# Optimization experiments

Measured on AMD Instinct MI355X. Metric: run time of the kernel, lower is better.

The kernel has to match this reference:

```python
import jax, jax.numpy as jnp
import numpy as np

N_HEADS = 16
N_KV_HEADS = 4
HEAD_DIM = 128  # n_embd // n_head = 2048 // 16
NEG_INF = -1e9


def setup_inputs() -> dict:
    key = jax.random.key(0)
    ks = jax.random.split(key, 4)
    B, T, C = 8, 1024, 2048
    x = jax.random.normal(ks[0], (B, T, C), dtype=jnp.float32)
    sc = 1.0 / np.sqrt(C)
    Wq = jax.random.normal(ks[1], (C, C), dtype=jnp.float32) * sc
    bq = jnp.zeros((C,), dtype=jnp.float32)
    Wkv = jax.random.normal(ks[2], (N_KV_HEADS * HEAD_DIM * 2, C), dtype=jnp.float32) * sc
    bkv = jnp.zeros((N_KV_HEADS * HEAD_DIM * 2,), dtype=jnp.float32)
    Wo = jax.random.normal(ks[3], (C, C), dtype=jnp.float32) * sc
    bo = jnp.zeros((C,), dtype=jnp.float32)
    return {"x": x, "Wq": Wq, "bq": bq, "Wkv": Wkv, "bkv": bkv, "Wo": Wo, "bo": bo}


def reference(x, Wq, bq, Wkv, bkv, Wo, bo):
    B, T, C = x.shape
    g = N_HEADS // N_KV_HEADS  # group size for repeat_interleave
    # q: [B, H, T, D]
    q = (x @ Wq.T + bq).reshape(B, T, N_HEADS, HEAD_DIM).transpose(0, 2, 1, 3)
    # kv: [B, T, Hkv, 2, D] -> [B, Hkv, T, 2, D]
    kv = (x @ Wkv.T + bkv).reshape(B, T, N_KV_HEADS, 2, HEAD_DIM).transpose(0, 2, 1, 3, 4)
    k = kv[..., 0, :]  # [B, Hkv, T, D]
    v = kv[..., 1, :]
    # repeat_interleave along head dim to expand kv heads to full heads
    k = jnp.repeat(k, g, axis=1)  # [B, H, T, D]
    v = jnp.repeat(v, g, axis=1)
    scale = 1.0 / jnp.sqrt(jnp.asarray(HEAD_DIM, dtype=x.dtype))
    scores = jnp.einsum('bhqd,bhkd->bhqk', q, k) * scale  # [B, H, T, T]
    causal = jnp.tril(jnp.ones((T, T), dtype=bool))
    scores = jnp.where(causal[None, None], scores, NEG_INF)
    attn = jax.nn.softmax(scores, axis=-1)
    y = jnp.einsum('bhqk,bhkd->bhqd', attn, v)  # [B, H, T, D]
    y = y.transpose(0, 2, 1, 3).reshape(B, T, C)
    return y @ Wo.T + bo
```

## Files before the change

kernel.cpp:

```cpp
#include <hip/hip_runtime.h>

typedef short short8 __attribute__((ext_vector_type(8)));
typedef short short4v __attribute__((ext_vector_type(4)));
typedef float floatx4 __attribute__((ext_vector_type(4)));
typedef unsigned short ushort_t;
typedef unsigned int uint_t;

#define DI __device__ __forceinline__

DI ushort_t f2bf(float f) {
  uint_t u = __builtin_bit_cast(uint_t, f);
  uint_t r = u + 0x7FFFu + ((u >> 16) & 1u);
  return (ushort_t)(r >> 16);
}

DI float exp2a(float x) {
  float r;
  asm("v_exp_f32 %0, %1" : "=v"(r) : "v"(x));
  return r;
}

DI floatx4 mfma16(short8 a, short8 b, floatx4 c) {
  return __builtin_amdgcn_mfma_f32_16x16x32_bf16(a, b, c, 0, 0, 0);
}

DI void async16(const void* g, void* l) {
  __builtin_amdgcn_global_load_lds(
      (__attribute__((address_space(1))) void*)(g),
      (__attribute__((address_space(3))) void*)(l), 16, 0, 0);
}

DI void cfence() { asm volatile("" ::: "memory"); }

__global__ __launch_bounds__(256)
void k_f2bf4(const float* __restrict__ x, const float* __restrict__ wq,
             const float* __restrict__ wkv, const float* __restrict__ wo,
             ushort_t* __restrict__ xb, ushort_t* __restrict__ wqb,
             ushort_t* __restrict__ wkvb, ushort_t* __restrict__ wob)
{
  const int blk = blockIdx.x;
  const float* in; ushort_t* out; long base;
  if (blk < 8192)       { in = x;   out = xb;   base = (long)blk * 2048; }
  else if (blk < 10240) { in = wq;  out = wqb;  base = (long)(blk - 8192) * 2048; }
  else if (blk < 11264) { in = wkv; out = wkvb; base = (long)(blk - 10240) * 2048; }
  else                  { in = wo;  out = wob;  base = (long)(blk - 11264) * 2048; }
  const long i = base + (long)threadIdx.x * 8;
  const float4 a = *(const float4*)(in + i);
  const float4 b = *(const float4*)(in + i + 4);
  union { short8 s; ushort_t u[8]; } o;
  o.u[0] = f2bf(a.x); o.u[1] = f2bf(a.y); o.u[2] = f2bf(a.z); o.u[3] = f2bf(a.w);
  o.u[4] = f2bf(b.x); o.u[5] = f2bf(b.y); o.u[6] = f2bf(b.z); o.u[7] = f2bf(b.w);
  *(short8*)(out + i) = o.s;
}

__global__ __launch_bounds__(256)
void k_gemmkv(const ushort_t* __restrict__ A, const ushort_t* __restrict__ B,
              const float* __restrict__ bias, ushort_t* __restrict__ KVout,
              ushort_t* __restrict__ Vt, int N, int K)
{
  __shared__ __align__(16) ushort_t As[4][128 * 32];
  __shared__ __align__(16) ushort_t Bs[4][128 * 32];
  const int tid = threadIdx.x;
  const int w = tid >> 6, l = tid & 63;
  const int wm = w >> 1, wn = w & 1;
  const int lr = l & 15, lg = l >> 4;
  const long m0 = (long)blockIdx.y * 128;
  const long n0 = (long)blockIdx.x * 128;

  const floatx4 fz = {0.f, 0.f, 0.f, 0.f};
  floatx4 acc[4][4];
#pragma unroll
  for (int i = 0; i < 4; ++i)
#pragma unroll
    for (int j = 0; j < 4; ++j) acc[i][j] = fz;

  const int c0 = tid, c1 = 256 + tid;
  const int r0 = c0 >> 2, r1 = c1 >> 2;
  const ushort_t* gA0 = A + (m0 + r0) * K + (((c0 & 3) ^ (r0 & 3)) << 3);
  const ushort_t* gA1 = A + (m0 + r1) * K + (((c1 & 3) ^ (r1 & 3)) << 3);
  const ushort_t* gB0 = B + (n0 + r0) * K + (((c0 & 3) ^ (r0 & 3)) << 3);
  const ushort_t* gB1 = B + (n0 + r1) * K + (((c1 & 3) ^ (r1 & 3)) << 3);

  const int nK = K >> 5;
#pragma unroll
  for (int pt = 0; pt < 3; ++pt) {
    const int ko = pt << 5;
    async16(gA0 + ko, &As[pt][c0 * 8]);
    async16(gA1 + ko, &As[pt][c1 * 8]);
    async16(gB0 + ko, &Bs[pt][c0 * 8]);
    async16(gB1 + ko, &Bs[pt][c1 * 8]);
  }

  const int xg = (lr & 3);

  for (int kt = 0; kt < nK; ++kt) {
    const int cur = kt & 3;
    const int rem = nK - 1 - kt;
    if (rem >= 3) {
      const int ko = (kt + 3) << 5;
      const int nb = (kt + 3) & 3;
      async16(gA0 + ko, &As[nb][c0 * 8]);
      async16(gA1 + ko, &As[nb][c1 * 8]);
      async16(gB0 + ko, &Bs[nb][c0 * 8]);
      async16(gB1 + ko, &Bs[nb][c1 * 8]);
      asm volatile("s_waitcnt vmcnt(12)" ::: "memory");
    } else if (rem == 2) {
      asm volatile("s_waitcnt vmcnt(8)" ::: "memory");
    } else if (rem == 1) {
      asm volatile("s_waitcnt vmcnt(4)" ::: "memory");
    } else {
      asm volatile("s_waitcnt vmcnt(0)" ::: "memory");
    }
    __builtin_amdgcn_s_barrier();
    cfence();

    short8 a[4], b[4];
#pragma unroll
    for (int i = 0; i < 4; ++i)
      a[i] = *(const short8*)&As[cur][(wm * 64 + i * 16 + lr) * 32 + ((lg ^ xg) * 8)];
#pragma unroll
    for (int j = 0; j < 4; ++j)
      b[j] = *(const short8*)&Bs[cur][(wn * 64 + j * 16 + lr) * 32 + ((lg ^ xg) * 8)];
#pragma unroll
    for (int i = 0; i < 4; ++i)
#pragma unroll
      for (int j = 0; j < 4; ++j)
        acc[i][j] = mfma16(a[i], b[j], acc[i][j]);

    asm volatile("s_waitcnt lgkmcnt(0)" ::: "memory");
    __builtin_amdgcn_s_barrier();
    cfence();
  }

#pragma unroll
  for (int j = 0; j < 4; ++j) {
    const long gn = n0 + wn * 64 + j * 16 + lr;
    const float bv = bias[gn];
    const int isV = (int)((gn >> 7) & 1);
    const long vrowB = (long)((gn >> 8) * 128 + (gn & 127)) * 1024;
#pragma unroll
    for (int i = 0; i < 4; ++i) {
      const long gm = m0 + wm * 64 + i * 16 + lg * 4;
#pragma unroll
      for (int r = 0; r < 4; ++r) {
        const ushort_t ov = f2bf(acc[i][j][r] + bv);
        const long gmr = gm + r;
        if (isV) Vt[((gmr >> 10) * 512) * 1024 + vrowB + (gmr & 1023)] = ov;
        else     KVout[gmr * 1024 + gn] = ov;
      }
    }
  }
}

template<int OUT_BF16>
__global__ __launch_bounds__(512, 4)
void k_gemm3(const ushort_t* __restrict__ A, const ushort_t* __restrict__ B,
             const float* __restrict__ bias, void* __restrict__ Cout,
             int N, int K, int gx, float out_scale)
{
  __shared__ __align__(16) ushort_t Al[2][256 * 32];
  __shared__ __align__(16) ushort_t Bl[2][128 * 32];
  const int tid = threadIdx.x;
  const int w = tid >> 6, l = tid & 63;
  const int wr = w >> 1, wc = w & 1;
  const int lr = l & 15, lg = l >> 4;

  const int nwg = gridDim.x;
  const int qd = nwg >> 3;
  const int p = blockIdx.x;
  const int swz = (p & 7) * qd + (p >> 3);
  const long m0 = (long)(swz / gx) * 256;
  const long n0 = (long)(swz % gx) * 128;

  const floatx4 fz = {0.f, 0.f, 0.f, 0.f};
  floatx4 acc[4][4];
#pragma unroll
  for (int i = 0; i < 4; ++i)
#pragma unroll
    for (int j = 0; j < 4; ++j) acc[i][j] = fz;

  const int cA0 = tid, cA1 = 512 + tid, cB = tid;
  const int rA0 = cA0 >> 2, rA1 = cA1 >> 2, rB = cB >> 2;
  const ushort_t* aS0 = A + (m0 + rA0) * K + (((cA0 & 3) ^ (rA0 & 3)) << 3);
  const ushort_t* aS1 = A + (m0 + rA1) * K + (((cA1 & 3) ^ (rA1 & 3)) << 3);
  const ushort_t* bS  = B + (n0 + rB) * K + (((cB & 3) ^ (rB & 3)) << 3);
  const int dA0 = cA0 * 8, dA1 = cA1 * 8, dB = cB * 8;

  const int xs = lg ^ (lr & 3);
  const int raB = (wr * 64 + lr) * 32 + xs * 8;
  const int rbB = (wc * 64 + lr) * 32 + xs * 8;

  const int nT = K >> 5;
  async16(aS0, &Al[0][dA0]);
  async16(aS1, &Al[0][dA1]);
  async16(bS,  &Bl[0][dB]);

  for (int t = 0; t < nT; ++t) {
    const int cur = t & 1;
    asm volatile("s_waitcnt vmcnt(0)" ::: "memory");
    asm volatile("s_waitcnt lgkmcnt(0)" ::: "memory");
    __builtin_amdgcn_s_barrier();
    cfence();
    if (t + 1 < nT) {
      const int ko = (t + 1) << 5;
      async16(aS0 + ko, &Al[cur ^ 1][dA0]);
      async16(aS1 + ko, &Al[cur ^ 1][dA1]);
      async16(bS + ko,  &Bl[cur ^ 1][dB]);
    }
    short8 a[4], b[4];
#pragma unroll
    for (int i = 0; i < 4; ++i)
      a[i] = *(const short8*)&Al[cur][raB + i * 512];
#pragma unroll
    for (int j = 0; j < 4; ++j)
      b[j] = *(const short8*)&Bl[cur][rbB + j * 512];
    __builtin_amdgcn_s_setprio(1);
#pragma unroll
    for (int i = 0; i < 4; ++i)
#pragma unroll
      for (int j = 0; j < 4; ++j)
        acc[i][j] = mfma16(a[i], b[j], acc[i][j]);
    __builtin_amdgcn_s_setprio(0);
    cfence();
  }

#pragma unroll
  for (int j = 0; j < 4; ++j) {
    const long gn = n0 + wc * 64 + j * 16 + lr;
    const float bv = bias[gn];
#pragma unroll
    for (int i = 0; i < 4; ++i) {
      const long gm = m0 + wr * 64 + i * 16 + lg * 4;
#pragma unroll
      for (int r = 0; r < 4; ++r) {
        const float v = (acc[i][j][r] + bv) * out_scale;
        if (OUT_BF16) ((ushort_t*)Cout)[(gm + r) * N + gn] = f2bf(v);
        else          ((float*)Cout)[(gm + r) * N + gn] = v;
      }
    }
  }
}

__global__ __launch_bounds__(256)
void k_attn(const ushort_t* __restrict__ Q, const ushort_t* __restrict__ KV,
            const ushort_t* __restrict__ Vt, ushort_t* __restrict__ Y)
{
  __shared__ __align__(16) ushort_t Kl[2][64 * 128];
  __shared__ __align__(16) ushort_t Vl[2][128 * 64];
  __shared__ __align__(16) ushort_t Pl[4][16][72];
  const int tid = threadIdx.x;
  const int w = tid >> 6, l = tid & 63;
  const int lr = l & 15, lg = l >> 4;
  const int p = blockIdx.x;
  const int v = ((p & 7) << 8) | (p >> 3);
  const int b = v >> 8;
  const int kh = (v >> 6) & 3;
  const int hs = (v >> 4) & 3;
  const int qt = 15 - (v & 15);
  const int h = kh * 4 + hs;
  const int qrow = qt * 64 + w * 16;

  const ushort_t* qptr = Q + ((long)(b * 1024 + qrow + lr)) * 2048 + h * 128 + lg * 8;
  short8 qf[4];
#pragma unroll
  for (int c = 0; c < 4; ++c) qf[c] = *(const short8*)(qptr + c * 32);

  const ushort_t* kg[4];
  const ushort_t* vg[4];
  int ld[4];
#pragma unroll
  for (int i = 0; i < 4; ++i) {
    const int c = i * 256 + tid;
    const int row = c >> 4, sgk = (c & 15) ^ (row & 7);
    kg[i] = KV + ((long)(b * 1024 + row)) * 1024 + kh * 256 + sgk * 8;
    const int d = c >> 3, sgv = (c & 7) ^ (d & 7);
    vg[i] = Vt + ((long)((b * 4 + kh) * 128 + d)) * 1024 + sgv * 8;
    ld[i] = c * 8;
  }

  float m_s = 0.f;
  float l_p = 0.f;
  const floatx4 fz = {0.f, 0.f, 0.f, 0.f};
  floatx4 yacc[8];
#pragma unroll
  for (int dt = 0; dt < 8; ++dt) yacc[dt] = fz;

  const int xk = (lr & 7) << 4;

#pragma unroll
  for (int i = 0; i < 4; ++i) async16(kg[i], &Kl[0][ld[i]]);
#pragma unroll
  for (int i = 0; i < 4; ++i) async16(vg[i], &Vl[0][ld[i]]);

  for (int t = 0; t <= qt; ++t) {
    const ushort_t* KlC = &Kl[t & 1][0];
    const ushort_t* VlC = &Vl[t & 1][0];
    asm volatile("s_waitcnt vmcnt(0)" ::: "memory");
    asm volatile("s_waitcnt lgkmcnt(0)" ::: "memory");
    __builtin_amdgcn_s_barrier();
    cfence();
    if (t < qt) {
      const long ko = (long)(t + 1) * 65536;
      const long vo = (long)(t + 1) * 64;
      ushort_t* KlN = &Kl[(t + 1) & 1][0];
      ushort_t* VlN = &Vl[(t + 1) & 1][0];
#pragma unroll
      for (int i = 0; i < 4; ++i) async16(kg[i] + ko, &KlN[ld[i]]);
#pragma unroll
      for (int i = 0; i < 4; ++i) async16(vg[i] + vo, &VlN[ld[i]]);
    }

    const floatx4 finit = {-m_s, -m_s, -m_s, -m_s};
    floatx4 st[4];
#pragma unroll
    for (int k2 = 0; k2 < 4; ++k2) {
      floatx4 sacc = finit;
      const int row = k2 * 16 + lr;
#pragma unroll
      for (int c = 0; c < 4; ++c) {
        const int off = row * 256 + ((c * 64 + lg * 16) ^ xk);
        const short8 kf = *(const short8*)((const char*)KlC + off);
        sacc = mfma16(kf, qf[c], sacc);
      }
      st[k2] = sacc;
    }
    if (t == qt) {
      const int qg = qrow + lr;
#pragma unroll
      for (int k2 = 0; k2 < 4; ++k2)
#pragma unroll
        for (int r = 0; r < 4; ++r)
          if (t * 64 + k2 * 16 + lg * 4 + r > qg) st[k2][r] = -__builtin_inff();
    }
    float pm = -__builtin_inff();
#pragma unroll
    for (int k2 = 0; k2 < 4; ++k2)
      pm = fmaxf(pm, fmaxf(fmaxf(st[k2][0], st[k2][1]), fmaxf(st[k2][2], st[k2][3])));
    if (!__all(pm <= 8.f)) {
      float pmf = fmaxf(pm, __shfl_xor(pm, 16));
      pmf = fmaxf(pmf, __shfl_xor(pmf, 32));
      const float d = fmaxf(pmf, 0.f);
      m_s += d;
      const float corr = exp2a(-d);
      l_p *= corr;
      const float cc0 = __shfl(corr, lg * 4 + 0);
      const float cc1 = __shfl(corr, lg * 4 + 1);
      const float cc2 = __shfl(corr, lg * 4 + 2);
      const float cc3 = __shfl(corr, lg * 4 + 3);
#pragma unroll
      for (int dt = 0; dt < 8; ++dt) {
        yacc[dt][0] *= cc0; yacc[dt][1] *= cc1;
        yacc[dt][2] *= cc2; yacc[dt][3] *= cc3;
      }
#pragma unroll
      for (int k2 = 0; k2 < 4; ++k2)
#pragma unroll
        for (int r = 0; r < 4; ++r) st[k2][r] -= d;
    }
    float psum = 0.f;
#pragma unroll
    for (int k2 = 0; k2 < 4; ++k2) {
      const float pe0 = exp2a(st[k2][0]);
      const float pe1 = exp2a(st[k2][1]);
      const float pe2 = exp2a(st[k2][2]);
      const float pe3 = exp2a(st[k2][3]);
      psum += (pe0 + pe1) + (pe2 + pe3);
      uint_t d0, d1;
      asm("v_cvt_pk_bf16_f32 %0, %1, %2" : "=v"(d0) : "v"(pe0), "v"(pe1));
      asm("v_cvt_pk_bf16_f32 %0, %1, %2" : "=v"(d1) : "v"(pe2), "v"(pe3));
      uint2 pkv; pkv.x = d0; pkv.y = d1;
      *(uint2*)&Pl[w][lr][k2 * 16 + lg * 4] = pkv;
    }
    l_p += psum;
    asm volatile("s_waitcnt lgkmcnt(0)" ::: "memory");

#pragma unroll
    for (int kc = 0; kc < 2; ++kc) {
      const short8 pf = *(const short8*)&Pl[w][lr][kc * 32 + lg * 8];
#pragma unroll
      for (int dt = 0; dt < 8; ++dt) {
        const int d = dt * 16 + lr;
        const int off = d * 128 + ((kc * 64 + lg * 16) ^ xk);
        const short8 vf = *(const short8*)((const char*)VlC + off);
        yacc[dt] = mfma16(pf, vf, yacc[dt]);
      }
    }
    cfence();
  }

  float l_s = l_p;
  l_s += __shfl_xor(l_s, 16);
  l_s += __shfl_xor(l_s, 32);
  const float linv = 1.f / l_s;
  const float i0 = __shfl(linv, lg * 4 + 0);
  const float i1 = __shfl(linv, lg * 4 + 1);
  const float i2 = __shfl(linv, lg * 4 + 2);
  const float i3 = __shfl(linv, lg * 4 + 3);
  ushort_t* yp = Y + ((long)(b * 1024 + qrow)) * 2048 + h * 128 + lr;
#pragma unroll
  for (int dt = 0; dt < 8; ++dt) {
    yp[(long)(lg * 4 + 0) * 2048 + dt * 16] = f2bf(yacc[dt][0] * i0);
    yp[(long)(lg * 4 + 1) * 2048 + dt * 16] = f2bf(yacc[dt][1] * i1);
    yp[(long)(lg * 4 + 2) * 2048 + dt * 16] = f2bf(yacc[dt][2] * i2);
    yp[(long)(lg * 4 + 3) * 2048 + dt * 16] = f2bf(yacc[dt][3] * i3);
  }
}

extern "C" void kernel_launch(void* const* d_in, const int* in_sizes, int n_in,
                              void* d_out, int out_size, void* d_ws, size_t ws_size,
                              hipStream_t stream)
{
  (void)in_sizes; (void)n_in; (void)out_size;
  const float* x   = (const float*)d_in[0];
  const float* Wq  = (const float*)d_in[1];
  const float* bq  = (const float*)d_in[2];
  const float* Wkv = (const float*)d_in[3];
  const float* bkv = (const float*)d_in[4];
  const float* Wo  = (const float*)d_in[5];
  const float* bo  = (const float*)d_in[6];
  float* out = (float*)d_out;
  char* ws = (char*)d_ws;

  if (ws_size < 104857600) return;

  ushort_t* xb   = (ushort_t*)(ws);
  ushort_t* Qb   = (ushort_t*)(ws + 33554432);
  ushort_t* KVb  = (ushort_t*)(ws + 67108864);
  ushort_t* Wqb  = (ushort_t*)(ws + 83886080);
  ushort_t* Wkvb = (ushort_t*)(ws + 92274688);
  ushort_t* Wob  = (ushort_t*)(ws + 96468992);
  ushort_t* Vtb  = Wqb;
  ushort_t* Yb   = xb;

  k_f2bf4<<<dim3(13312), 256, 0, stream>>>(x, Wq, Wkv, Wo, xb, Wqb, Wkvb, Wob);

  const float scale = 0.12751743f;
  k_gemm3<1><<<dim3(512), 512, 0, stream>>>(xb, Wqb, bq, Qb, 2048, 2048, 16, scale);
  k_gemmkv<<<dim3(8, 64), 256, 0, stream>>>(xb, Wkvb, bkv, KVb, Vtb, 1024, 2048);
  k_attn<<<dim3(2048), 256, 0, stream>>>(Qb, KVb, Vtb, Yb);
  k_gemm3<0><<<dim3(512), 512, 0, stream>>>(Yb, Wob, bo, out, 2048, 2048, 16, 1.0f);
}
```

Baseline: 318.8 us.

## Enlarge GEMM tiles to 256x256 with 64-wide K steps and 16 waves

Replaces the 256x128 GEMM tile (8 waves, K step 32) with a 256x256 tile handled by 16 waves per 1024-thread block, with a K step of 64 and an XOR swizzle widened to 8 chunks. Each tile now does twice the MFMA work per barrier and reuses more data per global load, while launching half as many workgroups (256). The cost is more LDS per block (128KB double-buffered), possibly lower occupancy, and fewer workgroups than twice the CU count, which can cause load imbalance. The two waitcnt instructions are also merged into one.

Measured after the change: 303.2 us, median of 2. 4.9% less time.

```diff
diff --git a/kernel.cpp b/kernel.cpp
--- a/kernel.cpp
+++ b/kernel.cpp
@@ -153,16 +153,16 @@
 }
 
 template<int OUT_BF16>
-__global__ __launch_bounds__(512, 4)
-void k_gemm3(const ushort_t* __restrict__ A, const ushort_t* __restrict__ B,
+__global__ __launch_bounds__(1024, 4)
+void k_gemm4(const ushort_t* __restrict__ A, const ushort_t* __restrict__ B,
              const float* __restrict__ bias, void* __restrict__ Cout,
              int N, int K, int gx, float out_scale)
 {
-  __shared__ __align__(16) ushort_t Al[2][256 * 32];
-  __shared__ __align__(16) ushort_t Bl[2][128 * 32];
+  __shared__ __align__(16) ushort_t Al[2][256 * 64];
+  __shared__ __align__(16) ushort_t Bl[2][256 * 64];
   const int tid = threadIdx.x;
   const int w = tid >> 6, l = tid & 63;
-  const int wr = w >> 1, wc = w & 1;
+  const int wrow = w >> 2, wcol = w & 3;
   const int lr = l & 15, lg = l >> 4;
 
   const int nwg = gridDim.x;
@@ -170,7 +170,7 @@
   const int p = blockIdx.x;
   const int swz = (p & 7) * qd + (p >> 3);
   const long m0 = (long)(swz / gx) * 256;
-  const long n0 = (long)(swz % gx) * 128;
+  const long n0 = (long)(swz % gx) * 256;
 
   const floatx4 fz = {0.f, 0.f, 0.f, 0.f};
   floatx4 acc[4][4];
@@ -179,41 +179,45 @@
 #pragma unroll
     for (int j = 0; j < 4; ++j) acc[i][j] = fz;
 
-  const int cA0 = tid, cA1 = 512 + tid, cB = tid;
-  const int rA0 = cA0 >> 2, rA1 = cA1 >> 2, rB = cB >> 2;
-  const ushort_t* aS0 = A + (m0 + rA0) * K + (((cA0 & 3) ^ (rA0 & 3)) << 3);
-  const ushort_t* aS1 = A + (m0 + rA1) * K + (((cA1 & 3) ^ (rA1 & 3)) << 3);
-  const ushort_t* bS  = B + (n0 + rB) * K + (((cB & 3) ^ (rB & 3)) << 3);
-  const int dA0 = cA0 * 8, dA1 = cA1 * 8, dB = cB * 8;
-
-  const int xs = lg ^ (lr & 3);
-  const int raB = (wr * 64 + lr) * 32 + xs * 8;
-  const int rbB = (wc * 64 + lr) * 32 + xs * 8;
-
-  const int nT = K >> 5;
-  async16(aS0, &Al[0][dA0]);
-  async16(aS1, &Al[0][dA1]);
-  async16(bS,  &Bl[0][dB]);
+  const int cA0 = tid, cA1 = 1024 + tid;
+  const int rA0 = cA0 >> 3, rA1 = cA1 >> 3;
+  const ushort_t* aS0 = A + (m0 + rA0) * K + (((cA0 & 7) ^ (rA0 & 7)) << 3);
+  const ushort_t* aS1 = A + (m0 + rA1) * K + (((cA1 & 7) ^ (rA1 & 7)) << 3);
+  const ushort_t* bS0 = B + (n0 + rA0) * K + (((cA0 & 7) ^ (rA0 & 7)) << 3);
+  const ushort_t* bS1 = B + (n0 + rA1) * K + (((cA1 & 7) ^ (rA1 & 7)) << 3);
+  const int d0 = cA0 * 8, d1 = cA1 * 8;
+
+  const int x8 = lr & 7;
+  const int g0 = (lg ^ x8) * 8;
+  const int g1 = ((4 + lg) ^ x8) * 8;
+  const int raB = (wrow * 64 + lr) * 64;
+  const int rbB = (wcol * 64 + lr) * 64;
+
+  const int nT = K >> 6;
+  async16(aS0, &Al[0][d0]);
+  async16(aS1, &Al[0][d1]);
+  async16(bS0, &Bl[0][d0]);
+  async16(bS1, &Bl[0][d1]);
 
   for (int t = 0; t < nT; ++t) {
     const int cur = t & 1;
-    asm volatile("s_waitcnt vmcnt(0)" ::: "memory");
-    asm volatile("s_waitcnt lgkmcnt(0)" ::: "memory");
+    asm volatile("s_waitcnt vmcnt(0) lgkmcnt(0)" ::: "memory");
     __builtin_amdgcn_s_barrier();
     cfence();
     if (t + 1 < nT) {
-      const int ko = (t + 1) << 5;
-      async16(aS0 + ko, &Al[cur ^ 1][dA0]);
-      async16(aS1 + ko, &Al[cur ^ 1][dA1]);
-      async16(bS + ko,  &Bl[cur ^ 1][dB]);
+      const int ko = (t + 1) << 6;
+      async16(aS0 + ko, &Al[cur ^ 1][d0]);
+      async16(aS1 + ko, &Al[cur ^ 1][d1]);
+      async16(bS0 + ko, &Bl[cur ^ 1][d0]);
+      async16(bS1 + ko, &Bl[cur ^ 1][d1]);
     }
     short8 a[4], b[4];
 #pragma unroll
     for (int i = 0; i < 4; ++i)
-      a[i] = *(const short8*)&Al[cur][raB + i * 512];
+      a[i] = *(const short8*)&Al[cur][raB + i * 1024 + g0];
 #pragma unroll
     for (int j = 0; j < 4; ++j)
-      b[j] = *(const short8*)&Bl[cur][rbB + j * 512];
+      b[j] = *(const short8*)&Bl[cur][rbB + j * 1024 + g0];
     __builtin_amdgcn_s_setprio(1);
 #pragma unroll
     for (int i = 0; i < 4; ++i)
@@ -221,16 +225,29 @@
       for (int j = 0; j < 4; ++j)
         acc[i][j] = mfma16(a[i], b[j], acc[i][j]);
     __builtin_amdgcn_s_setprio(0);
+#pragma unroll
+    for (int i = 0; i < 4; ++i)
+      a[i] = *(const short8*)&Al[cur][raB + i * 1024 + g1];
+#pragma unroll
+    for (int j = 0; j < 4; ++j)
+      b[j] = *(const short8*)&Bl[cur][rbB + j * 1024 + g1];
+    __builtin_amdgcn_s_setprio(1);
+#pragma unroll
+    for (int i = 0; i < 4; ++i)
+#pragma unroll
+      for (int j = 0; j < 4; ++j)
+        acc[i][j] = mfma16(a[i], b[j], acc[i][j]);
+    __builtin_amdgcn_s_setprio(0);
     cfence();
   }
 
 #pragma unroll
   for (int j = 0; j < 4; ++j) {
-    const long gn = n0 + wc * 64 + j * 16 + lr;
+    const long gn = n0 + wcol * 64 + j * 16 + lr;
     const float bv = bias[gn];
 #pragma unroll
     for (int i = 0; i < 4; ++i) {
-      const long gm = m0 + wr * 64 + i * 16 + lg * 4;
+      const long gm = m0 + wrow * 64 + i * 16 + lg * 4;
 #pragma unroll
       for (int r = 0; r < 4; ++r) {
         const float v = (acc[i][j][r] + bv) * out_scale;
@@ -295,8 +312,7 @@
   for (int t = 0; t <= qt; ++t) {
     const ushort_t* KlC = &Kl[t & 1][0];
     const ushort_t* VlC = &Vl[t & 1][0];
-    asm volatile("s_waitcnt vmcnt(0)" ::: "memory");
-    asm volatile("s_waitcnt lgkmcnt(0)" ::: "memory");
+    asm volatile("s_waitcnt vmcnt(0) lgkmcnt(0)" ::: "memory");
     __builtin_amdgcn_s_barrier();
     cfence();
     if (t < qt) {
@@ -435,8 +451,8 @@
   k_f2bf4<<<dim3(13312), 256, 0, stream>>>(x, Wq, Wkv, Wo, xb, Wqb, Wkvb, Wob);
 
   const float scale = 0.12751743f;
-  k_gemm3<1><<<dim3(512), 512, 0, stream>>>(xb, Wqb, bq, Qb, 2048, 2048, 16, scale);
+  k_gemm4<1><<<dim3(256), 1024, 0, stream>>>(xb, Wqb, bq, Qb, 2048, 2048, 8, scale);
   k_gemmkv<<<dim3(8, 64), 256, 0, stream>>>(xb, Wkvb, bkv, KVb, Vtb, 1024, 2048);
   k_attn<<<dim3(2048), 256, 0, stream>>>(Qb, KVb, Vtb, Yb);
-  k_gemm3<0><<<dim3(512), 512, 0, stream>>>(Yb, Wob, bo, out, 2048, 2048, 16, 1.0f);
-}
+  k_gemm4<0><<<dim3(256), 1024, 0, stream>>>(Yb, Wob, bo, out, 2048, 2048, 8, 1.0f);
+}
```
